# Optimization experiments

Measured on AMD Instinct MI355X. Metric: run time of the kernel, lower is better.

Reference implementation:

```python
import jax, jax.numpy as jnp
import numpy as np

GAMMA = 2.0  # init arg gamma
EPS = 1e-8   # torch F.cosine_similarity eps


def setup_inputs() -> dict:
    key = jax.random.key(0)
    k1, k2, k3 = jax.random.split(key, 3)
    B, C, H, W_ = 4, 256, 64, 64
    x = jax.random.normal(k1, (B, C, H, W_), dtype=jnp.float32)
    # 1x1 conv weight [out_c, in_c] and bias
    W = jax.random.normal(k2, (C, C), dtype=jnp.float32) * (1.0 / np.sqrt(C))
    b = jax.random.normal(k3, (C,), dtype=jnp.float32) * 0.01
    return {"x": x, "W": W, "b": b}


def reference(x, W, b):
    B, C, H, W_ = x.shape
    N = H * W_
    xf = x.reshape(B, C, N)                                    # [B,C,N]
    # cosine similarity across channel dim, with torch-style eps clamp
    norm = jnp.maximum(jnp.sqrt(jnp.sum(xf * xf, axis=1)), EPS)  # [B,N]
    xn = xf / norm[:, None, :]                                  # [B,C,N]
    sim = jnp.einsum('bcn,bcm->bnm', xn, xn)                    # [B,N,N]
    sim = jax.nn.relu(sim) ** GAMMA
    # 1x1 conv = per-pixel channel mixing
    t = jnp.einsum('oc,bchw->bohw', W, x) + b[None, :, None, None]
    tf = t.reshape(B, C, N)                                     # [B,C,N]
    # einsum 'b x y h w, b c h w -> b c x y'
    out = jnp.einsum('bnm,bcm->bcn', sim, tf)
    return out.reshape(B, C, H, W_)
```

## Files before the change

kernel.cpp:

```cpp
#include <hip/hip_runtime.h>
#include <stdint.h>

#define CC 256
#define NN 4096

typedef __attribute__((ext_vector_type(8))) short short8;
typedef __attribute__((ext_vector_type(4))) float floatx4;
typedef __attribute__((ext_vector_type(4))) unsigned int uint4v;
typedef __attribute__((ext_vector_type(2))) unsigned int uint2v;

__device__ __forceinline__ unsigned short f2bf(float f) {
    unsigned int u = __builtin_bit_cast(unsigned int, f);
    u = (u + 0x7FFFu + ((u >> 16) & 1u)) >> 16;
    return (unsigned short)u;
}

__device__ __forceinline__ floatx4 mfma16(short8 a, short8 b, floatx4 c) {
    return __builtin_amdgcn_mfma_f32_16x16x32_bf16(a, b, c, 0, 0, 0);
}


__global__ __launch_bounds__(256) void k_trans(const float* __restrict__ x,
                                               unsigned short* __restrict__ xB,
                                               unsigned short* __restrict__ xG,
                                               float* __restrict__ psum) {
    int blk = blockIdx.x;
    int b  = blk >> 8;
    int cc = (blk >> 6) & 3;
    int nc = blk & 63;
    int c0 = cc << 6, n0 = nc << 6;
    __shared__ float tile[64][65];
    __shared__ float red[4][64];
    int t = threadIdx.x;
    {
        int c   = t >> 2;
        int nn4 = (t & 3) << 4;
        const float* src = x + (size_t)(b * CC + c0 + c) * NN + n0 + nn4;
        #pragma unroll
        for (int j = 0; j < 16; j += 4) {
            floatx4 v = *(const floatx4*)(src + j);
            tile[c][nn4 + j + 0] = v[0];
            tile[c][nn4 + j + 1] = v[1];
            tile[c][nn4 + j + 2] = v[2];
            tile[c][nn4 + j + 3] = v[3];
        }
    }
    __syncthreads();
    int g = t >> 6, lane = t & 63, l15 = lane & 15, q = lane >> 4;
    #pragma unroll
    for (int kkl = 0; kkl < 2; ++kkl) {
        unsigned int w[4];
        #pragma unroll
        for (int j = 0; j < 4; ++j) {
            unsigned int lo = f2bf(tile[32 * kkl + 8 * q + 2 * j][16 * g + l15]);
            unsigned int hi = f2bf(tile[32 * kkl + 8 * q + 2 * j + 1][16 * g + l15]);
            w[j] = lo | (hi << 16);
        }
        uint4v p = {w[0], w[1], w[2], w[3]};
        *(uint4v*)(xB + ((size_t)(b * 256 + (n0 >> 4) + g) * 8 + (c0 >> 5) + kkl) * 512
                   + lane * 8) = p;
    }
    #pragma unroll
    for (int kk2 = 0; kk2 < 2; ++kk2) {
        unsigned int w[4];
        #pragma unroll
        for (int j = 0; j < 4; ++j) {
            unsigned int lo = f2bf(tile[16 * g + l15][32 * kk2 + 8 * q + 2 * j]);
            unsigned int hi = f2bf(tile[16 * g + l15][32 * kk2 + 8 * q + 2 * j + 1]);
            w[j] = lo | (hi << 16);
        }
        uint4v p = {w[0], w[1], w[2], w[3]};
        *(uint4v*)(xG + (size_t)(b * 64 + nc) * 16 * 1024
                   + ((size_t)((c0 >> 4) + g)) * 1024 + kk2 * 512 + lane * 8) = p;
    }
    {
        int n  = t & 63;
        int cq = t >> 6;
        float ss = 0.f;
        #pragma unroll
        for (int i = 0; i < 16; ++i) {
            float v = tile[cq * 16 + i][n];
            ss = fmaf(v, v, ss);
        }
        red[cq][n] = ss;
    }
    __syncthreads();
    if (t < 64) {
        float s = red[0][t] + red[1][t] + red[2][t] + red[3][t];
        psum[((size_t)(b * 64 + nc) * 64 + t) * 4 + cc] = s;
    }
}

__global__ __launch_bounds__(256) void k_invwcast(const float* __restrict__ psum,
                                                  float* __restrict__ invn,
                                                  const float* __restrict__ Wm,
                                                  unsigned short* __restrict__ wF) {
    int bid = blockIdx.x;
    int t = threadIdx.x;
    if (bid < 64) {
        int i = bid * 256 + t;
        floatx4 p = *(const floatx4*)(psum + (size_t)i * 4);
        float ss = (p[0] + p[1]) + (p[2] + p[3]);
        invn[i] = 1.f / fmaxf(sqrtf(ss), 1e-8f);
    } else {
        int idx = (bid - 64) * 256 + t;
        int f = idx >> 6, lane = idx & 63;
        int ct = f >> 3, kk = f & 7;
        int l15 = lane & 15, q = lane >> 4;
        const float* src = Wm + (size_t)(16 * ct + l15) * CC + 32 * kk + 8 * q;
        floatx4 a = *(const floatx4*)src;
        floatx4 c = *(const floatx4*)(src + 4);
        unsigned int w0 = f2bf(a[0]) | ((unsigned int)f2bf(a[1]) << 16);
        unsigned int w1 = f2bf(a[2]) | ((unsigned int)f2bf(a[3]) << 16);
        unsigned int w2 = f2bf(c[0]) | ((unsigned int)f2bf(c[1]) << 16);
        unsigned int w3 = f2bf(c[2]) | ((unsigned int)f2bf(c[3]) << 16);
        uint4v p = {w0, w1, w2, w3};
        *(uint4v*)(wF + (size_t)f * 512 + lane * 8) = p;
    }
}

#define FUSED_STEP(IT, BQC, BQN, XGP, XGC, DO_G2)                              \
    {                                                                          \
                \
        _Pragma("unroll")                                                      \
        for (int kk = 0; kk < 8; ++kk)                                         \
            BQN[kk] = *(const short8*)(bqp + kk * 512);                        \
        bqp += 16384;                                                          \
        _Pragma("unroll")                                                      \
        for (int ci = 0; ci < 2; ++ci)                                         \
            _Pragma("unroll")                                                  \
            for (int kk2 = 0; kk2 < 2; ++kk2)                                  \
                XGC[ci][kk2] = *(const short8*)(xgp + ci * 8192 + kk2 * 512);  \
        xgp += 16384;                                                          \
        floatx4 invm4 = *(const floatx4*)invmp;                                \
        invmp += 64;                                                           \
                                       \
        if (DO_G2) {                                                           \
            const unsigned short* pbR = pbuf[((IT) - 1) & 1];                  \
            _Pragma("unroll")                                                  \
            for (int kk2 = 0; kk2 < 2; ++kk2)                                  \
                _Pragma("unroll")                                              \
                for (int nqs = 0; nqs < 4; ++nqs) {                            \
                    short8 pbf = *(const short8*)(pbR + (16 * nqs + l15) * 72  \
                                                  + kk2 * 32 + q * 8);         \
                    Zacc[0][nqs] = mfma16(XGP[0][kk2], pbf, Zacc[0][nqs]);     \
                    Zacc[1][nqs] = mfma16(XGP[1][kk2], pbf, Zacc[1][nqs]);     \
                }                                                              \
        }                                                                      \
                  \
        floatx4 s0a = zero4, s0b = zero4, s1a = zero4, s1b = zero4;            \
        _Pragma("unroll")                                                      \
        for (int kk = 0; kk < 8; kk += 2) {                                    \
            s0a = mfma16(BQC[kk],     aq[0][kk],     s0a);                     \
            s1a = mfma16(BQC[kk],     aq[1][kk],     s1a);                     \
            s0b = mfma16(BQC[kk + 1], aq[0][kk + 1], s0b);                     \
            s1b = mfma16(BQC[kk + 1], aq[1][kk + 1], s1b);                     \
        }                                                                      \
                  \
        {                                                                      \
            unsigned short* pbW = pbuf[(IT) & 1];                              \
            _Pragma("unroll")                                                  \
            for (int s = 0; s < 2; ++s) {                                      \
                floatx4 sv = (s == 0) ? (s0a + s0b) : (s1a + s1b);             \
                unsigned int pk0, pk1;                                         \
                float v0 = sv[0] * (invm4[0] * invq[s]);                       \
                float v1 = sv[1] * (invm4[1] * invq[s]);                       \
                float v2 = sv[2] * (invm4[2] * invq[s]);                       \
                float v3 = sv[3] * (invm4[3] * invq[s]);                       \
                v0 = fmaxf(v0, 0.f); v1 = fmaxf(v1, 0.f);                      \
                v2 = fmaxf(v2, 0.f); v3 = fmaxf(v3, 0.f);                      \
                v0 *= v0; v1 *= v1; v2 *= v2; v3 *= v3;                        \
                csum[s] += (v0 + v1) + (v2 + v3);                              \
                pk0 = __byte_perm(__builtin_bit_cast(unsigned int, v0) + 0x8000u, \
                                  __builtin_bit_cast(unsigned int, v1) + 0x8000u, \
                                  0x7632);                                     \
                pk1 = __byte_perm(__builtin_bit_cast(unsigned int, v2) + 0x8000u, \
                                  __builtin_bit_cast(unsigned int, v3) + 0x8000u, \
                                  0x7632);                                     \
                uint2v w2 = {pk0, pk1};                                        \
                *(uint2v*)(pbW + (16 * (2 * np + s) + l15) * 72                \
                           + 16 * ms + 4 * q) = w2;                            \
            }                                                                  \
        }                                                                      \
        asm volatile("s_waitcnt lgkmcnt(0)\n\ts_barrier" ::: "memory");        \
    }

__global__ __launch_bounds__(512, 1) void k_fused(
        const unsigned short* __restrict__ xB,
        const unsigned short* __restrict__ xG,
        const unsigned short* __restrict__ wF,
        const float* __restrict__ bias,
        const float* __restrict__ invn,
        float* __restrict__ out) {
    int blk = blockIdx.x;
    int b  = blk >> 6;
    int n0 = (blk & 63) << 6;
    int t  = threadIdx.x;
    int wv = t >> 6, lane = t & 63;
    int l15 = lane & 15, q = lane >> 4;
    int ms = wv & 3;
    int np = wv >> 2;

    __shared__ unsigned short pbuf[2][64 * 72];
    __shared__ unsigned short zbuf[64 * 264];
    __shared__ float spbuf2[4][64];

    const unsigned short* xBb = xB + (size_t)b * 256 * 8 * 512;
    const unsigned short* xGb = xG + (size_t)b * 64 * 16 * 1024;
    const float* invb = invn + b * NN;

    short8 aq[2][8];
    #pragma unroll
    for (int s = 0; s < 2; ++s)
        #pragma unroll
        for (int kk = 0; kk < 8; ++kk)
            aq[s][kk] = *(const short8*)(xBb
                + ((size_t)((n0 >> 4) + 2 * np + s) * 8 + kk) * 512 + lane * 8);
    float invq[2];
    #pragma unroll
    for (int s = 0; s < 2; ++s) invq[s] = invb[n0 + 16 * (2 * np + s) + l15];

    floatx4 zero4 = {0.f, 0.f, 0.f, 0.f};
    floatx4 Zacc[2][4];
    #pragma unroll
    for (int ci = 0; ci < 2; ++ci)
        #pragma unroll
        for (int nqs = 0; nqs < 4; ++nqs) Zacc[ci][nqs] = zero4;
    float csum[2] = {0.f, 0.f};

    const unsigned short* bqp   = xBb + ms * 4096 + lane * 8;
    const unsigned short* xgp   = xGb + wv * 1024 + lane * 8;
    const float*          invmp = invb + 16 * ms + 4 * q;

    short8 bqA[8], bqB[8];
    short8 xgA[2][2], xgB[2][2];
    #pragma unroll
    for (int kk = 0; kk < 8; ++kk)
        bqA[kk] = *(const short8*)(bqp + kk * 512);
    bqp += 16384;

    FUSED_STEP(0, bqA, bqB, xgB, xgA, false)
    for (int it2 = 0; it2 < 31; ++it2) {
        int itO = 2 * it2 + 1;
        FUSED_STEP(itO, bqB, bqA, xgA, xgB, true)
        int itE = 2 * it2 + 2;
        FUSED_STEP(itE, bqA, bqB, xgB, xgA, true)
    }
    FUSED_STEP(63, bqB, bqA, xgA, xgB, true)
    {
        const unsigned short* pbR = pbuf[1];
        #pragma unroll
        for (int kk2 = 0; kk2 < 2; ++kk2)
            #pragma unroll
            for (int nqs = 0; nqs < 4; ++nqs) {
                short8 pbf = *(const short8*)(pbR + (16 * nqs + l15) * 72
                                              + kk2 * 32 + q * 8);
                Zacc[0][nqs] = mfma16(xgB[0][kk2], pbf, Zacc[0][nqs]);
                Zacc[1][nqs] = mfma16(xgB[1][kk2], pbf, Zacc[1][nqs]);
            }
    }

    #pragma unroll
    for (int s = 0; s < 2; ++s) {
        csum[s] += __shfl_xor(csum[s], 16, 64);
        csum[s] += __shfl_xor(csum[s], 32, 64);
    }

    __syncthreads();
    #pragma unroll
    for (int ci = 0; ci < 2; ++ci) {
        int cct = wv + 8 * ci;
        #pragma unroll
        for (int nqs = 0; nqs < 4; ++nqs)
            #pragma unroll
            for (int i = 0; i < 4; ++i)
                zbuf[(16 * nqs + l15) * 264 + 16 * cct + 4 * q + i] = f2bf(Zacc[ci][nqs][i]);
    }
    if (q == 0) {
        #pragma unroll
        for (int s = 0; s < 2; ++s)
            spbuf2[ms][16 * (2 * np + s) + l15] = csum[s];
    }
    __syncthreads();

    float svals[4];
    #pragma unroll
    for (int nqs = 0; nqs < 4; ++nqs)
        svals[nqs] = spbuf2[0][16 * nqs + l15] + spbuf2[1][16 * nqs + l15]
                   + spbuf2[2][16 * nqs + l15] + spbuf2[3][16 * nqs + l15];

    float* ob = out + (size_t)b * CC * NN;
    floatx4 oa[2][4];
    #pragma unroll
    for (int ci = 0; ci < 2; ++ci) {
        int ct = wv + 8 * ci;
        floatx4 bv = *(const floatx4*)(bias + 16 * ct + 4 * q);
        #pragma unroll
        for (int nqs = 0; nqs < 4; ++nqs)
            #pragma unroll
            for (int i = 0; i < 4; ++i) oa[ci][nqs][i] = bv[i] * svals[nqs];
    }
    #pragma unroll
    for (int kk = 0; kk < 8; ++kk) {
        short8 wf0 = *(const short8*)(wF + (size_t)(wv * 8 + kk) * 512 + lane * 8);
        short8 wf1 = *(const short8*)(wF + (size_t)((wv + 8) * 8 + kk) * 512 + lane * 8);
        #pragma unroll
        for (int nqs = 0; nqs < 4; ++nqs) {
            short8 zf = *(const short8*)(&zbuf[(16 * nqs + l15) * 264 + 32 * kk + 8 * q]);
            oa[0][nqs] = mfma16(wf0, zf, oa[0][nqs]);
            oa[1][nqs] = mfma16(wf1, zf, oa[1][nqs]);
        }
    }
    #pragma unroll
    for (int ci = 0; ci < 2; ++ci) {
        int ct = wv + 8 * ci;
        #pragma unroll
        for (int nqs = 0; nqs < 4; ++nqs)
            #pragma unroll
            for (int i = 0; i < 4; ++i)
                ob[(size_t)(16 * ct + 4 * q + i) * NN + n0 + 16 * nqs + l15] = oa[ci][nqs][i];
    }
}

extern "C" void kernel_launch(void* const* d_in, const int* in_sizes, int n_in,
                              void* d_out, int out_size, void* d_ws, size_t ws_size,
                              hipStream_t stream) {
    const float* x    = (const float*)d_in[0];
    const float* Wm   = (const float*)d_in[1];
    const float* bias = (const float*)d_in[2];
    float* out = (float*)d_out;

    char* ws = (char*)d_ws;
    float* psum         = (float*)ws;
    float* invn         = (float*)(ws + 262144);
    unsigned short* xB  = (unsigned short*)(ws + 262144 + 65536);
    unsigned short* xG  = (unsigned short*)(ws + 262144 + 65536 + 8388608);
    unsigned short* wF  = (unsigned short*)(ws + 262144 + 65536 + 2 * 8388608);

    k_trans   <<<1024, 256, 0, stream>>>(x, xB, xG, psum);
    k_invwcast<<<96,   256, 0, stream>>>(psum, invn, Wm, wF);
    k_fused   <<<256,  512, 0, stream>>>(xB, xG, wF, bias, invn, out);
}
```

Measured before the change: 152.3 us.

## Halve fused-kernel query tile to 32 with 4-wave blocks and 512-block grid

The fused attention-like kernel now processes 32 query pixels per block with 256 threads instead of 64 with 512, launching 512 blocks at two per CU. Each wave now computes four channel tiles for the second GEMM. The xG loads are made local to each step and the second MFMA group is moved after the similarity MFMAs. Block indices are remapped so neighbouring blocks share a batch. The aim is more blocks and better CU load balance on a 256-CU part, at the cost of reloading the key (bq) stream twice as often per query pixel and losing the xG register prefetch.

```diff
diff --git a/kernel.cpp b/kernel.cpp
--- a/kernel.cpp
+++ b/kernel.cpp
@@ -119,34 +119,25 @@
     }
 }
 
-#define FUSED_STEP(IT, BQC, BQN, XGP, XGC, DO_G2)                              \
+#define FUSED_STEP(IT, BQC, BQN, DO_G2)                                        \
     {                                                                          \
-                \
+                                                      \
         _Pragma("unroll")                                                      \
         for (int kk = 0; kk < 8; ++kk)                                         \
             BQN[kk] = *(const short8*)(bqp + kk * 512);                        \
         bqp += 16384;                                                          \
-        _Pragma("unroll")                                                      \
-        for (int ci = 0; ci < 2; ++ci)                                         \
+                                    \
+        short8 xgv[4][2];                                                      \
+        if (DO_G2) {                                                           \
             _Pragma("unroll")                                                  \
-            for (int kk2 = 0; kk2 < 2; ++kk2)                                  \
-                XGC[ci][kk2] = *(const short8*)(xgp + ci * 8192 + kk2 * 512);  \
-        xgp += 16384;                                                          \
+            for (int ci = 0; ci < 4; ++ci)                                     \
+                _Pragma("unroll")                                              \
+                for (int kk2 = 0; kk2 < 2; ++kk2)                              \
+                    xgv[ci][kk2] = *(const short8*)(xgp + ci * 4096 + kk2 * 512); \
+            xgp += 16384;                                                      \
+        }                                                                      \
         floatx4 invm4 = *(const floatx4*)invmp;                                \
         invmp += 64;                                                           \
-                                       \
-        if (DO_G2) {                                                           \
-            const unsigned short* pbR = pbuf[((IT) - 1) & 1];                  \
-            _Pragma("unroll")                                                  \
-            for (int kk2 = 0; kk2 < 2; ++kk2)                                  \
-                _Pragma("unroll")                                              \
-                for (int nqs = 0; nqs < 4; ++nqs) {                            \
-                    short8 pbf = *(const short8*)(pbR + (16 * nqs + l15) * 72  \
-                                                  + kk2 * 32 + q * 8);         \
-                    Zacc[0][nqs] = mfma16(XGP[0][kk2], pbf, Zacc[0][nqs]);     \
-                    Zacc[1][nqs] = mfma16(XGP[1][kk2], pbf, Zacc[1][nqs]);     \
-                }                                                              \
-        }                                                                      \
                   \
         floatx4 s0a = zero4, s0b = zero4, s1a = zero4, s1b = zero4;            \
         _Pragma("unroll")                                                      \
@@ -155,6 +146,20 @@
             s1a = mfma16(BQC[kk],     aq[1][kk],     s1a);                     \
             s0b = mfma16(BQC[kk + 1], aq[0][kk + 1], s0b);                     \
             s1b = mfma16(BQC[kk + 1], aq[1][kk + 1], s1b);                     \
+        }                                                                      \
+                                   \
+        if (DO_G2) {                                                           \
+            const unsigned short* pbR = pbuf[((IT) - 1) & 1];                  \
+            _Pragma("unroll")                                                  \
+            for (int kk2 = 0; kk2 < 2; ++kk2)                                  \
+                _Pragma("unroll")                                              \
+                for (int nqs = 0; nqs < 2; ++nqs) {                            \
+                    short8 pbf = *(const short8*)(pbR + (16 * nqs + l15) * 72  \
+                                                  + kk2 * 32 + q * 8);         \
+                    _Pragma("unroll")                                          \
+                    for (int ci = 0; ci < 4; ++ci)                             \
+                        Zacc[ci][nqs] = mfma16(xgv[ci][kk2], pbf, Zacc[ci][nqs]); \
+                }                                                              \
         }                                                                      \
                   \
         {                                                                      \
@@ -178,14 +183,13 @@
                                   __builtin_bit_cast(unsigned int, v3) + 0x8000u, \
                                   0x7632);                                     \
                 uint2v w2 = {pk0, pk1};                                        \
-                *(uint2v*)(pbW + (16 * (2 * np + s) + l15) * 72                \
-                           + 16 * ms + 4 * q) = w2;                            \
+                *(uint2v*)(pbW + (16 * s + l15) * 72 + 16 * ms + 4 * q) = w2;  \
             }                                                                  \
         }                                                                      \
         asm volatile("s_waitcnt lgkmcnt(0)\n\ts_barrier" ::: "memory");        \
     }
 
-__global__ __launch_bounds__(512, 1) void k_fused(
+__global__ __launch_bounds__(256, 2) void k_fused(
         const unsigned short* __restrict__ xB,
         const unsigned short* __restrict__ xG,
         const unsigned short* __restrict__ wF,
@@ -193,17 +197,17 @@
         const float* __restrict__ invn,
         float* __restrict__ out) {
     int blk = blockIdx.x;
-    int b  = blk >> 6;
-    int n0 = (blk & 63) << 6;
+    int b  = (blk & 7) >> 1;
+    int qt = ((blk >> 3) << 1) | (blk & 1);
+    int n0 = qt << 5;
     int t  = threadIdx.x;
     int wv = t >> 6, lane = t & 63;
     int l15 = lane & 15, q = lane >> 4;
-    int ms = wv & 3;
-    int np = wv >> 2;
-
-    __shared__ unsigned short pbuf[2][64 * 72];
-    __shared__ unsigned short zbuf[64 * 264];
-    __shared__ float spbuf2[4][64];
+    int ms = wv;
+
+    __shared__ unsigned short pbuf[2][32 * 72];
+    __shared__ unsigned short zbuf[32 * 264];
+    __shared__ float spbuf2[4][32];
 
     const unsigned short* xBb = xB + (size_t)b * 256 * 8 * 512;
     const unsigned short* xGb = xG + (size_t)b * 64 * 16 * 1024;
@@ -215,17 +219,17 @@
         #pragma unroll
         for (int kk = 0; kk < 8; ++kk)
             aq[s][kk] = *(const short8*)(xBb
-                + ((size_t)((n0 >> 4) + 2 * np + s) * 8 + kk) * 512 + lane * 8);
+                + ((size_t)((n0 >> 4) + s) * 8 + kk) * 512 + lane * 8);
     float invq[2];
     #pragma unroll
-    for (int s = 0; s < 2; ++s) invq[s] = invb[n0 + 16 * (2 * np + s) + l15];
+    for (int s = 0; s < 2; ++s) invq[s] = invb[n0 + 16 * s + l15];
 
     floatx4 zero4 = {0.f, 0.f, 0.f, 0.f};
-    floatx4 Zacc[2][4];
-    #pragma unroll
-    for (int ci = 0; ci < 2; ++ci)
-        #pragma unroll
-        for (int nqs = 0; nqs < 4; ++nqs) Zacc[ci][nqs] = zero4;
+    floatx4 Zacc[4][2];
+    #pragma unroll
+    for (int ci = 0; ci < 4; ++ci)
+        #pragma unroll
+        for (int nqs = 0; nqs < 2; ++nqs) Zacc[ci][nqs] = zero4;
     float csum[2] = {0.f, 0.f};
 
     const unsigned short* bqp   = xBb + ms * 4096 + lane * 8;
@@ -233,30 +237,34 @@
     const float*          invmp = invb + 16 * ms + 4 * q;
 
     short8 bqA[8], bqB[8];
-    short8 xgA[2][2], xgB[2][2];
     #pragma unroll
     for (int kk = 0; kk < 8; ++kk)
         bqA[kk] = *(const short8*)(bqp + kk * 512);
     bqp += 16384;
 
-    FUSED_STEP(0, bqA, bqB, xgB, xgA, false)
+    FUSED_STEP(0, bqA, bqB, false)
     for (int it2 = 0; it2 < 31; ++it2) {
-        int itO = 2 * it2 + 1;
-        FUSED_STEP(itO, bqB, bqA, xgA, xgB, true)
-        int itE = 2 * it2 + 2;
-        FUSED_STEP(itE, bqA, bqB, xgB, xgA, true)
-    }
-    FUSED_STEP(63, bqB, bqA, xgA, xgB, true)
+        FUSED_STEP(2 * it2 + 1, bqB, bqA, true)
+        FUSED_STEP(2 * it2 + 2, bqA, bqB, true)
+    }
+    FUSED_STEP(63, bqB, bqA, true)
     {
+        short8 xgv[4][2];
+        #pragma unroll
+        for (int ci = 0; ci < 4; ++ci)
+            #pragma unroll
+            for (int kk2 = 0; kk2 < 2; ++kk2)
+                xgv[ci][kk2] = *(const short8*)(xgp + ci * 4096 + kk2 * 512);
         const unsigned short* pbR = pbuf[1];
         #pragma unroll
         for (int kk2 = 0; kk2 < 2; ++kk2)
             #pragma unroll
-            for (int nqs = 0; nqs < 4; ++nqs) {
+            for (int nqs = 0; nqs < 2; ++nqs) {
                 short8 pbf = *(const short8*)(pbR + (16 * nqs + l15) * 72
                                               + kk2 * 32 + q * 8);
-                Zacc[0][nqs] = mfma16(xgB[0][kk2], pbf, Zacc[0][nqs]);
-                Zacc[1][nqs] = mfma16(xgB[1][kk2], pbf, Zacc[1][nqs]);
+                #pragma unroll
+                for (int ci = 0; ci < 4; ++ci)
+                    Zacc[ci][nqs] = mfma16(xgv[ci][kk2], pbf, Zacc[ci][nqs]);
             }
     }
 
@@ -268,10 +276,10 @@
 
     __syncthreads();
     #pragma unroll
-    for (int ci = 0; ci < 2; ++ci) {
-        int cct = wv + 8 * ci;
-        #pragma unroll
-        for (int nqs = 0; nqs < 4; ++nqs)
+    for (int ci = 0; ci < 4; ++ci) {
+        int cct = wv + 4 * ci;
+        #pragma unroll
+        for (int nqs = 0; nqs < 2; ++nqs)
             #pragma unroll
             for (int i = 0; i < 4; ++i)
                 zbuf[(16 * nqs + l15) * 264 + 16 * cct + 4 * q + i] = f2bf(Zacc[ci][nqs][i]);
@@ -279,43 +287,46 @@
     if (q == 0) {
         #pragma unroll
         for (int s = 0; s < 2; ++s)
-            spbuf2[ms][16 * (2 * np + s) + l15] = csum[s];
+            spbuf2[ms][16 * s + l15] = csum[s];
     }
     __syncthreads();
 
-    float svals[4];
-    #pragma unroll
-    for (int nqs = 0; nqs < 4; ++nqs)
+    float svals[2];
+    #pragma unroll
+    for (int nqs = 0; nqs < 2; ++nqs)
         svals[nqs] = spbuf2[0][16 * nqs + l15] + spbuf2[1][16 * nqs + l15]
                    + spbuf2[2][16 * nqs + l15] + spbuf2[3][16 * nqs + l15];
 
     float* ob = out + (size_t)b * CC * NN;
-    floatx4 oa[2][4];
-    #pragma unroll
-    for (int ci = 0; ci < 2; ++ci) {
-        int ct = wv + 8 * ci;
+    floatx4 oa[4][2];
+    #pragma unroll
+    for (int ci = 0; ci < 4; ++ci) {
+        int ct = wv + 4 * ci;
         floatx4 bv = *(const floatx4*)(bias + 16 * ct + 4 * q);
         #pragma unroll
-        for (int nqs = 0; nqs < 4; ++nqs)
+        for (int nqs = 0; nqs < 2; ++nqs)
             #pragma unroll
             for (int i = 0; i < 4; ++i) oa[ci][nqs][i] = bv[i] * svals[nqs];
     }
     #pragma unroll
     for (int kk = 0; kk < 8; ++kk) {
-        short8 wf0 = *(const short8*)(wF + (size_t)(wv * 8 + kk) * 512 + lane * 8);
-        short8 wf1 = *(const short8*)(wF + (size_t)((wv + 8) * 8 + kk) * 512 + lane * 8);
-        #pragma unroll
-        for (int nqs = 0; nqs < 4; ++nqs) {
+        short8 wf[4];
+        #pragma unroll
+        for (int ci = 0; ci < 4; ++ci)
+            wf[ci] = *(const short8*)(wF + (size_t)((wv + 4 * ci) * 8 + kk) * 512 + lane * 8);
+        #pragma unroll
+        for (int nqs = 0; nqs < 2; ++nqs) {
             short8 zf = *(const short8*)(&zbuf[(16 * nqs + l15) * 264 + 32 * kk + 8 * q]);
-            oa[0][nqs] = mfma16(wf0, zf, oa[0][nqs]);
-            oa[1][nqs] = mfma16(wf1, zf, oa[1][nqs]);
-        }
-    }
-    #pragma unroll
-    for (int ci = 0; ci < 2; ++ci) {
-        int ct = wv + 8 * ci;
-        #pragma unroll
-        for (int nqs = 0; nqs < 4; ++nqs)
+            #pragma unroll
+            for (int ci = 0; ci < 4; ++ci)
+                oa[ci][nqs] = mfma16(wf[ci], zf, oa[ci][nqs]);
+        }
+    }
+    #pragma unroll
+    for (int ci = 0; ci < 4; ++ci) {
+        int ct = wv + 4 * ci;
+        #pragma unroll
+        for (int nqs = 0; nqs < 2; ++nqs)
             #pragma unroll
             for (int i = 0; i < 4; ++i)
                 ob[(size_t)(16 * ct + 4 * q + i) * NN + n0 + 16 * nqs + l15] = oa[ci][nqs][i];
@@ -339,5 +350,5 @@
 
     k_trans   <<<1024, 256, 0, stream>>>(x, xB, xG, psum);
     k_invwcast<<<96,   256, 0, stream>>>(psum, invn, Wm, wF);
-    k_fused   <<<256,  512, 0, stream>>>(xB, xG, wF, bias, invn, out);
-}
+    k_fused   <<<512,  256, 0, stream>>>(xB, xG, wF, bias, invn, out);
+}
```

Measured after the change: 163.9 us. 1.08x slower.

## Stage shared key tiles in LDS via direct global-to-LDS loads and reorder blocks

Applied to the files above, without the earlier changes.

Each key tile is now loaded once per block with global_load_lds into a double-buffered LDS array, and every wave reads its slice from LDS. Previously each wave pulled its tile straight into registers, so waves sharing the same ms index fetched the same data. This removes that redundant global traffic and frees many VGPRs. The barrier now waits with vmcnt so the prefetch overlaps the next step, the inverse-norm load is double-buffered, and the similarity MFMAs are moved ahead of the G2 MFMAs under raised wave priority. The block index is also remapped to interleave batches. The last iteration prefetches past the end of the buffers, a small out-of-bounds read.

```diff
diff --git a/kernel.cpp b/kernel.cpp
--- a/kernel.cpp
+++ b/kernel.cpp
@@ -119,22 +119,45 @@
     }
 }
 
-#define FUSED_STEP(IT, BQC, BQN, XGP, XGC, DO_G2)                              \
+#define FUSED_STEP(IT, XGP, XGC, INVP, INVC, DO_G2)                            \
     {                                                                          \
-                \
+             \
+                                        \
         _Pragma("unroll")                                                      \
-        for (int kk = 0; kk < 8; ++kk)                                         \
-            BQN[kk] = *(const short8*)(bqp + kk * 512);                        \
-        bqp += 16384;                                                          \
+        for (int i = 0; i < 4; ++i)                                            \
+            __builtin_amdgcn_global_load_lds(                                  \
+                (const __attribute__((address_space(1))) unsigned int*)        \
+                    (const void*)(bqsrc + i * 512),                            \
+                (__attribute__((address_space(3))) unsigned int*)              \
+                    (void*)(bqlds[((IT) + 1) & 1] + wv * 2048 + i * 512),      \
+                16, 0, 0);                                                     \
+        bqsrc += 16384;                                                        \
+        asm volatile("" ::: "memory");                                        \
+                        \
         _Pragma("unroll")                                                      \
         for (int ci = 0; ci < 2; ++ci)                                         \
             _Pragma("unroll")                                                  \
             for (int kk2 = 0; kk2 < 2; ++kk2)                                  \
                 XGC[ci][kk2] = *(const short8*)(xgp + ci * 8192 + kk2 * 512);  \
         xgp += 16384;                                                          \
-        floatx4 invm4 = *(const floatx4*)invmp;                                \
+        INVC = *(const floatx4*)invmp;                                         \
         invmp += 64;                                                           \
-                                       \
+                                \
+        short8 bq0[8];                                                         \
+        _Pragma("unroll")                                                      \
+        for (int kk = 0; kk < 8; ++kk)                                         \
+            bq0[kk] = *(const short8*)(bqlds[(IT) & 1] + ms * 4096 + kk * 512  \
+                                       + lane * 8);                            \
+        __builtin_amdgcn_s_setprio(1);                                         \
+        floatx4 s0a = zero4, s0b = zero4, s1a = zero4, s1b = zero4;            \
+        _Pragma("unroll")                                                      \
+        for (int kk = 0; kk < 8; kk += 2) {                                    \
+            s0a = mfma16(bq0[kk],     aq[0][kk],     s0a);                     \
+            s1a = mfma16(bq0[kk],     aq[1][kk],     s1a);                     \
+            s0b = mfma16(bq0[kk + 1], aq[0][kk + 1], s0b);                     \
+            s1b = mfma16(bq0[kk + 1], aq[1][kk + 1], s1b);                     \
+        }                                                                      \
+                     \
         if (DO_G2) {                                                           \
             const unsigned short* pbR = pbuf[((IT) - 1) & 1];                  \
             _Pragma("unroll")                                                  \
@@ -147,15 +170,7 @@
                     Zacc[1][nqs] = mfma16(XGP[1][kk2], pbf, Zacc[1][nqs]);     \
                 }                                                              \
         }                                                                      \
-                  \
-        floatx4 s0a = zero4, s0b = zero4, s1a = zero4, s1b = zero4;            \
-        _Pragma("unroll")                                                      \
-        for (int kk = 0; kk < 8; kk += 2) {                                    \
-            s0a = mfma16(BQC[kk],     aq[0][kk],     s0a);                     \
-            s1a = mfma16(BQC[kk],     aq[1][kk],     s1a);                     \
-            s0b = mfma16(BQC[kk + 1], aq[0][kk + 1], s0b);                     \
-            s1b = mfma16(BQC[kk + 1], aq[1][kk + 1], s1b);                     \
-        }                                                                      \
+        __builtin_amdgcn_s_setprio(0);                                         \
                   \
         {                                                                      \
             unsigned short* pbW = pbuf[(IT) & 1];                              \
@@ -163,10 +178,10 @@
             for (int s = 0; s < 2; ++s) {                                      \
                 floatx4 sv = (s == 0) ? (s0a + s0b) : (s1a + s1b);             \
                 unsigned int pk0, pk1;                                         \
-                float v0 = sv[0] * (invm4[0] * invq[s]);                       \
-                float v1 = sv[1] * (invm4[1] * invq[s]);                       \
-                float v2 = sv[2] * (invm4[2] * invq[s]);                       \
-                float v3 = sv[3] * (invm4[3] * invq[s]);                       \
+                float v0 = sv[0] * (INVP[0] * invq[s]);                        \
+                float v1 = sv[1] * (INVP[1] * invq[s]);                        \
+                float v2 = sv[2] * (INVP[2] * invq[s]);                        \
+                float v3 = sv[3] * (INVP[3] * invq[s]);                        \
                 v0 = fmaxf(v0, 0.f); v1 = fmaxf(v1, 0.f);                      \
                 v2 = fmaxf(v2, 0.f); v3 = fmaxf(v3, 0.f);                      \
                 v0 *= v0; v1 *= v1; v2 *= v2; v3 *= v3;                        \
@@ -182,7 +197,8 @@
                            + 16 * ms + 4 * q) = w2;                            \
             }                                                                  \
         }                                                                      \
-        asm volatile("s_waitcnt lgkmcnt(0)\n\ts_barrier" ::: "memory");        \
+            \
+        asm volatile("s_waitcnt vmcnt(5) lgkmcnt(0)\n\ts_barrier" ::: "memory"); \
     }
 
 __global__ __launch_bounds__(512, 1) void k_fused(
@@ -193,14 +209,16 @@
         const float* __restrict__ invn,
         float* __restrict__ out) {
     int blk = blockIdx.x;
-    int b  = blk >> 6;
-    int n0 = (blk & 63) << 6;
+    int b  = (blk & 7) >> 1;
+    int qt = ((blk >> 3) << 1) | (blk & 1);
+    int n0 = qt << 6;
     int t  = threadIdx.x;
     int wv = t >> 6, lane = t & 63;
     int l15 = lane & 15, q = lane >> 4;
     int ms = wv & 3;
     int np = wv >> 2;
 
+    __shared__ unsigned short bqlds[2][16384];
     __shared__ unsigned short pbuf[2][64 * 72];
     __shared__ unsigned short zbuf[64 * 264];
     __shared__ float spbuf2[4][64];
@@ -208,6 +226,20 @@
     const unsigned short* xBb = xB + (size_t)b * 256 * 8 * 512;
     const unsigned short* xGb = xG + (size_t)b * 64 * 16 * 1024;
     const float* invb = invn + b * NN;
+
+    const unsigned short* bqsrc = xBb + wv * 2048 + lane * 8;
+    const unsigned short* xgp   = xGb + wv * 1024 + lane * 8;
+    const float*          invmp = invb + 16 * ms + 4 * q;
+
+    #pragma unroll
+    for (int i = 0; i < 4; ++i)
+        __builtin_amdgcn_global_load_lds(
+            (const __attribute__((address_space(1))) unsigned int*)
+                (const void*)(bqsrc + i * 512),
+            (__attribute__((address_space(3))) unsigned int*)
+                (void*)(bqlds[0] + wv * 2048 + i * 512),
+            16, 0, 0);
+    bqsrc += 16384;
 
     short8 aq[2][8];
     #pragma unroll
@@ -228,25 +260,20 @@
         for (int nqs = 0; nqs < 4; ++nqs) Zacc[ci][nqs] = zero4;
     float csum[2] = {0.f, 0.f};
 
-    const unsigned short* bqp   = xBb + ms * 4096 + lane * 8;
-    const unsigned short* xgp   = xGb + wv * 1024 + lane * 8;
-    const float*          invmp = invb + 16 * ms + 4 * q;
-
-    short8 bqA[8], bqB[8];
     short8 xgA[2][2], xgB[2][2];
-    #pragma unroll
-    for (int kk = 0; kk < 8; ++kk)
-        bqA[kk] = *(const short8*)(bqp + kk * 512);
-    bqp += 16384;
-
-    FUSED_STEP(0, bqA, bqB, xgB, xgA, false)
+    floatx4 invA, invB;
+    invA = *(const floatx4*)invmp;
+    invmp += 64;
+
+    asm volatile("s_waitcnt vmcnt(0)" ::: "memory");
+    __syncthreads();
+
+    FUSED_STEP(0, xgB, xgA, invA, invB, false)
     for (int it2 = 0; it2 < 31; ++it2) {
-        int itO = 2 * it2 + 1;
-        FUSED_STEP(itO, bqB, bqA, xgA, xgB, true)
-        int itE = 2 * it2 + 2;
-        FUSED_STEP(itE, bqA, bqB, xgB, xgA, true)
-    }
-    FUSED_STEP(63, bqB, bqA, xgA, xgB, true)
+        FUSED_STEP(2 * it2 + 1, xgA, xgB, invB, invA, true)
+        FUSED_STEP(2 * it2 + 2, xgB, xgA, invA, invB, true)
+    }
+    FUSED_STEP(63, xgA, xgB, invB, invA, true)
     {
         const unsigned short* pbR = pbuf[1];
         #pragma unroll
```

Result: slower. 186.3 us (+22.3%).

## Split fused attention over key halves with atomic accumulation into zeroed output

Applied to the files above, without the earlier changes.

The key/pixel dimension m is split into two halves, so the fused kernel launches 512 blocks instead of 256. Each block processes 32 key tiles and adds its partial result into the output with atomicAdd. A new zeroing kernel clears the output first. The block index mapping is changed to interleave batches, the per-step inverse-norm loads are double-buffered, and the similarity MFMAs are moved ahead of the previous-step G2 MFMAs. The aim is to occupy more of the machine and hide latency better, at the cost of an extra zeroing pass and atomic read-modify-write traffic on the output.

```diff
diff --git a/kernel.cpp b/kernel.cpp
--- a/kernel.cpp
+++ b/kernel.cpp
@@ -19,6 +19,14 @@
     return __builtin_amdgcn_mfma_f32_16x16x32_bf16(a, b, c, 0, 0, 0);
 }
 
+
+__global__ __launch_bounds__(256) void k_zero(float* __restrict__ out) {
+    floatx4 z = {0.f, 0.f, 0.f, 0.f};
+    size_t base = ((size_t)blockIdx.x * 256 + threadIdx.x) * 4;
+    #pragma unroll
+    for (int j = 0; j < 4; ++j)
+        *(floatx4*)(out + base + (size_t)j * 1048576) = z;
+}
 
 __global__ __launch_bounds__(256) void k_trans(const float* __restrict__ x,
                                                unsigned short* __restrict__ xB,
@@ -119,22 +127,32 @@
     }
 }
 
-#define FUSED_STEP(IT, BQC, BQN, XGP, XGC, DO_G2)                              \
+#define FUSED_STEP(IT, BQC, BQN, XGP, XGC, INVP, INVC, DO_G2)                  \
     {                                                                          \
-                \
+                                                      \
         _Pragma("unroll")                                                      \
         for (int kk = 0; kk < 8; ++kk)                                         \
             BQN[kk] = *(const short8*)(bqp + kk * 512);                        \
         bqp += 16384;                                                          \
+                        \
         _Pragma("unroll")                                                      \
         for (int ci = 0; ci < 2; ++ci)                                         \
             _Pragma("unroll")                                                  \
             for (int kk2 = 0; kk2 < 2; ++kk2)                                  \
                 XGC[ci][kk2] = *(const short8*)(xgp + ci * 8192 + kk2 * 512);  \
         xgp += 16384;                                                          \
-        floatx4 invm4 = *(const floatx4*)invmp;                                \
+        INVC = *(const floatx4*)invmp;                                         \
         invmp += 64;                                                           \
-                                       \
+                  \
+        floatx4 s0a = zero4, s0b = zero4, s1a = zero4, s1b = zero4;            \
+        _Pragma("unroll")                                                      \
+        for (int kk = 0; kk < 8; kk += 2) {                                    \
+            s0a = mfma16(BQC[kk],     aq[0][kk],     s0a);                     \
+            s1a = mfma16(BQC[kk],     aq[1][kk],     s1a);                     \
+            s0b = mfma16(BQC[kk + 1], aq[0][kk + 1], s0b);                     \
+            s1b = mfma16(BQC[kk + 1], aq[1][kk + 1], s1b);                     \
+        }                                                                      \
+                     \
         if (DO_G2) {                                                           \
             const unsigned short* pbR = pbuf[((IT) - 1) & 1];                  \
             _Pragma("unroll")                                                  \
@@ -148,25 +166,16 @@
                 }                                                              \
         }                                                                      \
                   \
-        floatx4 s0a = zero4, s0b = zero4, s1a = zero4, s1b = zero4;            \
-        _Pragma("unroll")                                                      \
-        for (int kk = 0; kk < 8; kk += 2) {                                    \
-            s0a = mfma16(BQC[kk],     aq[0][kk],     s0a);                     \
-            s1a = mfma16(BQC[kk],     aq[1][kk],     s1a);                     \
-            s0b = mfma16(BQC[kk + 1], aq[0][kk + 1], s0b);                     \
-            s1b = mfma16(BQC[kk + 1], aq[1][kk + 1], s1b);                     \
-        }                                                                      \
-                  \
         {                                                                      \
             unsigned short* pbW = pbuf[(IT) & 1];                              \
             _Pragma("unroll")                                                  \
             for (int s = 0; s < 2; ++s) {                                      \
                 floatx4 sv = (s == 0) ? (s0a + s0b) : (s1a + s1b);             \
                 unsigned int pk0, pk1;                                         \
-                float v0 = sv[0] * (invm4[0] * invq[s]);                       \
-                float v1 = sv[1] * (invm4[1] * invq[s]);                       \
-                float v2 = sv[2] * (invm4[2] * invq[s]);                       \
-                float v3 = sv[3] * (invm4[3] * invq[s]);                       \
+                float v0 = sv[0] * (INVP[0] * invq[s]);                        \
+                float v1 = sv[1] * (INVP[1] * invq[s]);                        \
+                float v2 = sv[2] * (INVP[2] * invq[s]);                        \
+                float v3 = sv[3] * (INVP[3] * invq[s]);                        \
                 v0 = fmaxf(v0, 0.f); v1 = fmaxf(v1, 0.f);                      \
                 v2 = fmaxf(v2, 0.f); v3 = fmaxf(v3, 0.f);                      \
                 v0 *= v0; v1 *= v1; v2 *= v2; v3 *= v3;                        \
@@ -185,7 +194,7 @@
         asm volatile("s_waitcnt lgkmcnt(0)\n\ts_barrier" ::: "memory");        \
     }
 
-__global__ __launch_bounds__(512, 1) void k_fused(
+__global__ __launch_bounds__(512, 4) void k_fused(
         const unsigned short* __restrict__ xB,
         const unsigned short* __restrict__ xG,
         const unsigned short* __restrict__ wF,
@@ -193,8 +202,11 @@
         const float* __restrict__ invn,
         float* __restrict__ out) {
     int blk = blockIdx.x;
-    int b  = blk >> 6;
-    int n0 = (blk & 63) << 6;
+    int b  = (blk & 7) >> 1;
+    int r  = ((blk >> 3) << 1) | (blk & 1);
+    int qt = r >> 1;
+    int h  = r & 1;
+    int n0 = qt << 6;
     int t  = threadIdx.x;
     int wv = t >> 6, lane = t & 63;
     int l15 = lane & 15, q = lane >> 4;
@@ -228,25 +240,26 @@
         for (int nqs = 0; nqs < 4; ++nqs) Zacc[ci][nqs] = zero4;
     float csum[2] = {0.f, 0.f};
 
-    const unsigned short* bqp   = xBb + ms * 4096 + lane * 8;
-    const unsigned short* xgp   = xGb + wv * 1024 + lane * 8;
-    const float*          invmp = invb + 16 * ms + 4 * q;
+    const unsigned short* bqp   = xBb + (size_t)h * 524288 + ms * 4096 + lane * 8;
+    const unsigned short* xgp   = xGb + (size_t)h * 524288 + wv * 1024 + lane * 8;
+    const float*          invmp = invb + h * 2048 + 16 * ms + 4 * q;
 
     short8 bqA[8], bqB[8];
     short8 xgA[2][2], xgB[2][2];
+    floatx4 invA, invB;
     #pragma unroll
     for (int kk = 0; kk < 8; ++kk)
         bqA[kk] = *(const short8*)(bqp + kk * 512);
     bqp += 16384;
-
-    FUSED_STEP(0, bqA, bqB, xgB, xgA, false)
-    for (int it2 = 0; it2 < 31; ++it2) {
-        int itO = 2 * it2 + 1;
-        FUSED_STEP(itO, bqB, bqA, xgA, xgB, true)
-        int itE = 2 * it2 + 2;
-        FUSED_STEP(itE, bqA, bqB, xgB, xgA, true)
-    }
-    FUSED_STEP(63, bqB, bqA, xgA, xgB, true)
+    invA = *(const floatx4*)invmp;
+    invmp += 64;
+
+    FUSED_STEP(0, bqA, bqB, xgB, xgA, invA, invB, false)
+    for (int it2 = 0; it2 < 15; ++it2) {
+        FUSED_STEP(2 * it2 + 1, bqB, bqA, xgA, xgB, invB, invA, true)
+        FUSED_STEP(2 * it2 + 2, bqA, bqB, xgB, xgA, invA, invB, true)
+    }
+    FUSED_STEP(31, bqB, bqA, xgA, xgB, invB, invA, true)
     {
         const unsigned short* pbR = pbuf[1];
         #pragma unroll
@@ -318,7 +331,8 @@
         for (int nqs = 0; nqs < 4; ++nqs)
             #pragma unroll
             for (int i = 0; i < 4; ++i)
-                ob[(size_t)(16 * ct + 4 * q + i) * NN + n0 + 16 * nqs + l15] = oa[ci][nqs][i];
+                atomicAdd(&ob[(size_t)(16 * ct + 4 * q + i) * NN + n0 + 16 * nqs + l15],
+                          oa[ci][nqs][i]);
     }
 }
 
@@ -337,7 +351,8 @@
     unsigned short* xG  = (unsigned short*)(ws + 262144 + 65536 + 8388608);
     unsigned short* wF  = (unsigned short*)(ws + 262144 + 65536 + 2 * 8388608);
 
+    k_zero    <<<1024, 256, 0, stream>>>(out);
     k_trans   <<<1024, 256, 0, stream>>>(x, xB, xG, psum);
     k_invwcast<<<96,   256, 0, stream>>>(psum, invn, Wm, wF);
-    k_fused   <<<256,  512, 0, stream>>>(xB, xG, wF, bias, invn, out);
-}
+    k_fused   <<<512,  512, 0, stream>>>(xB, xG, wF, bias, invn, out);
+}
```

Result: slower. 363.2 us (+138.5%).
